# Kernel optimization log

Hardware: AMD Instinct MI355X
Metric: run time of the kernel (lower is better)

Reference implementation:

```python
import jax, jax.numpy as jnp
import numpy as np

N, E, D, R = 50000, 800000, 64, 65


def setup_inputs() -> dict:
    key = jax.random.key(0)
    ks = jax.random.split(key, 8)
    x = jax.random.normal(ks[0], (N, D), dtype=jnp.float32)
    src = jax.random.randint(ks[1], (E,), 0, N, dtype=jnp.int32)
    dst = jax.random.randint(ks[2], (E,), 0, N, dtype=jnp.int32)
    edge_type = jax.random.randint(ks[3], (E,), 0, R, dtype=jnp.int32)
    s = 1.0 / np.sqrt(D)
    W1 = jax.random.normal(ks[4], (R, D, D), dtype=jnp.float32) * s
    Wl1 = jax.random.normal(ks[5], (D, D), dtype=jnp.float32) * s
    W2 = jax.random.normal(ks[6], (R, D, D), dtype=jnp.float32) * s
    Wl2 = jax.random.normal(ks[7], (D, D), dtype=jnp.float32) * s
    return {"x": x, "src": src, "dst": dst, "edge_type": edge_type,
            "W1": W1, "Wl1": Wl1, "W2": W2, "Wl2": Wl2}


def _rgcn_layer(x, src, dst, edge_type, W, Wl):
    # x: [N, D_in], W: [R, D_in, D_out], Wl: [D_in, D_out]
    n = x.shape[0]
    r = W.shape[0]
    # per-relation transform of all node features: [R, N, D_out]
    xw = jnp.einsum('nd,rdh->rnh', x, W)
    # gather transformed source feature for each edge by its relation: [E, D_out]
    msg = xw[edge_type, src]
    # mean aggregation per (destination node, relation) as in PyG RGCNConv
    key = dst.astype(jnp.int32) * r + edge_type
    cnt = jax.ops.segment_sum(jnp.ones(key.shape, x.dtype), key, num_segments=n * r)
    norm = 1.0 / jnp.maximum(cnt[key], 1.0)  # [E]
    agg = jax.ops.segment_sum(msg * norm[:, None], dst, num_segments=n)  # [N, D_out]
    # self-loop linear term (self_loop_weights in original module)
    out = agg + x @ Wl
    # activation; dropout is identity in eval mode; batch norm disabled
    return jax.nn.relu(out)


def reference(x, src, dst, edge_type, W1, Wl1, W2, Wl2):
    h = _rgcn_layer(x, src, dst, edge_type, W1, Wl1)
    h = _rgcn_layer(h, src, dst, edge_type, W2, Wl2)
    return h
```

## Files before the change

kernel.cpp:

```cpp
#include <hip/hip_runtime.h>

typedef __attribute__((ext_vector_type(8))) short bf16x8;
typedef __attribute__((ext_vector_type(4))) float f32x4;

constexpr int D = 64;
constexpr int SEG = 64;
constexpr int CSTR = 16;
constexpr int TSTR = 68;

__device__ inline unsigned short f2bf(float f) {
  unsigned u = __float_as_uint(f);
  u += 0x7fff + ((u >> 16) & 1);
  return (unsigned short)(u >> 16);
}
__device__ inline float bflo(unsigned u) { return __uint_as_float(u << 16); }
__device__ inline float bfhi(unsigned u) { return __uint_as_float(u & 0xffff0000u); }

__global__ __launch_bounds__(256) void count_kernel(
    const int* __restrict__ dst, const int* __restrict__ et,
    int* __restrict__ bcnt, int* __restrict__ deg, int E, int R, int nbE) {
  __shared__ int lh[128];
  int t = threadIdx.x;
  if (t < 128) lh[t] = 0;
  __syncthreads();
  int e = blockIdx.x * 256 + t;
  if (e < E) {
    atomicAdd(&deg[(long)dst[e] * CSTR], 1);
    atomicAdd(&lh[et[e]], 1);
  }
  __syncthreads();
  if (t < R) bcnt[t * nbE + blockIdx.x] = lh[t];
}

__global__ __launch_bounds__(256) void scanA_dual_kernel(
    const int* __restrict__ bcnt, const int* __restrict__ deg,
    int* __restrict__ bsum, int nBC, int N, int nbBC) {
  __shared__ int s[256];
  int t = threadIdx.x;
  int b = blockIdx.x;
  int v;
  if (b < nbBC) {
    int i = b * 256 + t;
    v = (i < nBC) ? bcnt[i] : 0;
  } else {
    int i = (b - nbBC) * 256 + t;
    v = (i < N) ? deg[(long)i * CSTR] : 0;
  }
  s[t] = v;
  __syncthreads();
  for (int o = 128; o > 0; o >>= 1) {
    if (t < o) s[t] += s[t + o];
    __syncthreads();
  }
  if (t == 0) bsum[b] = s[0];
}

__device__ inline void scanB_region(int* bsum, int nb, int t) {
  __shared__ int s[256];
  __shared__ int carry;
  if (t == 0) carry = 0;
  __syncthreads();
  for (int base = 0; base < nb; base += 256) {
    int i = base + t;
    int v = (i < nb) ? bsum[i] : 0;
    s[t] = v;
    __syncthreads();
    for (int o = 1; o < 256; o <<= 1) {
      int u = (t >= o) ? s[t - o] : 0;
      __syncthreads();
      s[t] += u;
      __syncthreads();
    }
    if (i < nb) bsum[i] = carry + s[t] - v;
    __syncthreads();
    if (t == 0) carry += s[255];
    __syncthreads();
  }
}

__global__ __launch_bounds__(256) void scanB_dual_kernel(
    int* __restrict__ bsum, int nbBC, int nbN) {
  int t = threadIdx.x;
  scanB_region(bsum, nbBC, t);
  scanB_region(bsum + nbBC, nbN, t);
}

__global__ __launch_bounds__(256) void scanC_dual_kernel(
    const int* __restrict__ bcnt, const int* __restrict__ deg,
    const int* __restrict__ bsum, int* __restrict__ prefE,
    int* __restrict__ dstoff, int* __restrict__ cur2,
    int nBC, int N, int nbBC) {
  __shared__ int s[256];
  int t = threadIdx.x;
  int b = blockIdx.x;
  bool isBC = (b < nbBC);
  int i = (isBC ? b : b - nbBC) * 256 + t;
  int n = isBC ? nBC : N;
  int v = 0;
  if (i < n) v = isBC ? bcnt[i] : deg[(long)i * CSTR];
  s[t] = v;
  __syncthreads();
  for (int o = 1; o < 256; o <<= 1) {
    int u = (t >= o) ? s[t - o] : 0;
    __syncthreads();
    s[t] += u;
    __syncthreads();
  }
  int excl = bsum[b] + s[t] - v;
  if (isBC) {
    if (i < n) prefE[i] = excl;
    if (i == n - 1) prefE[n] = excl + v;
  } else {
    if (i < n) { dstoff[i] = excl; cur2[(long)i * CSTR] = excl; }
    if (i == n - 1) dstoff[n] = excl + v;
  }
}

__global__ void prefix_wrel_kernel(const int* __restrict__ prefE,
                                   int* __restrict__ cursor, int* __restrict__ wrel,
                                   int nbE, int R) {
  __shared__ int sc[128];
  int l = threadIdx.x;
  int c = 0;
  if (l < R) {
    int tot = prefE[(l + 1) * nbE] - prefE[l * nbE];
    c = (tot + SEG - 1) & ~(SEG - 1);
  }
  sc[l] = c;
  __syncthreads();
  for (int ofs = 1; ofs < 128; ofs <<= 1) {
    int v = (l >= ofs) ? sc[l - ofs] : 0;
    __syncthreads();
    sc[l] += v;
    __syncthreads();
  }
  if (l < R) {
    int cur = sc[l] - c;
    cursor[l] = cur;
    int w0 = cur >> 6;
    int nw = c >> 6;
    for (int w = 0; w < nw; ++w) wrel[w0 + w] = l;
  }
}

__global__ __launch_bounds__(256) void scatter_kernel(
    const int* __restrict__ src, const int* __restrict__ dst, const int* __restrict__ et,
    const int* __restrict__ cursor, const int* __restrict__ prefE,
    int* __restrict__ cur2, int2* __restrict__ eidx,
    int E, int R, int nbE) {
  __shared__ int lh[128];
  __shared__ int lbase[128];
  int t = threadIdx.x, b = blockIdx.x;
  if (t < R) {
    lh[t] = 0;
    lbase[t] = cursor[t] + prefE[t * nbE + b] - prefE[t * nbE];
  }
  __syncthreads();
  int e = b * 256 + t;
  if (e < E) {
    int r = et[e], s = src[e], d = dst[e];
    int lr = atomicAdd(&lh[r], 1);
    int jd = atomicAdd(&cur2[(long)d * CSTR], 1);
    int pos = lbase[r] + lr;
    eidx[pos] = make_int2(s, jd);
  }
}

__global__ __launch_bounds__(256) void cvt_all_kernel(
    const float* __restrict__ x, unsigned short* __restrict__ xb, int nx,
    const float* __restrict__ W1, unsigned short* __restrict__ WT1,
    const float* __restrict__ W2, unsigned short* __restrict__ WT2, int nw,
    const float* __restrict__ Wl1, unsigned short* __restrict__ WTl1,
    const float* __restrict__ Wl2, unsigned short* __restrict__ WTl2, int nl) {
  int i = blockIdx.x * 256 + threadIdx.x;
  if (i < nx) { xb[i] = f2bf(x[i]); return; }
  i -= nx;
  if (i < 2 * nw) {
    const float* W = (i < nw) ? W1 : W2;
    unsigned short* WT = (i < nw) ? WT1 : WT2;
    int i2 = (i < nw) ? i : i - nw;
    int n = i2 & 63, k = (i2 >> 6) & 63, r = i2 >> 12;
    WT[(r << 12) + (n << 6) + k] = f2bf(W[(r << 12) + (k << 6) + n]);
    return;
  }
  i -= 2 * nw;
  if (i < 2 * nl) {
    const float* W = (i < nl) ? Wl1 : Wl2;
    unsigned short* WT = (i < nl) ? WTl1 : WTl2;
    int i2 = (i < nl) ? i : i - nl;
    int n = i2 & 63, k = (i2 >> 6) & 63;
    WT[(n << 6) + k] = f2bf(W[(k << 6) + n]);
  }
}

__global__ __launch_bounds__(256) __attribute__((amdgpu_waves_per_eu(1, 4)))
void msg_kernel(const unsigned short* __restrict__ xb,
                const unsigned short* __restrict__ WT,
                const int2* __restrict__ eidx, const int* __restrict__ wrel,
                unsigned int* __restrict__ msgp, int* __restrict__ relrow, int nwaves) {
  const int lane = (int)threadIdx.x & 63;
  const int l15 = lane & 15;
  const int q = lane >> 4;
  const int wave = blockIdx.x * 4 + ((int)threadIdx.x >> 6);
  if (wave >= nwaves) return;
  const long base = (long)wave * SEG;
  const int r = wrel[wave];
  const unsigned short* wb = WT + ((long)r << 12);
  bf16x8 Bf[4][2];
#pragma unroll
  for (int nt = 0; nt < 4; ++nt)
#pragma unroll
    for (int kh = 0; kh < 2; ++kh)
      Bf[nt][kh] = *(const bf16x8*)(wb + (nt * 16 + l15) * 64 + kh * 32 + q * 8);
#pragma unroll
  for (int t = 0; t < 4; ++t) {
    int2 rec = eidx[base + t * 16 + l15];
    if (relrow && lane < 16 && rec.y >= 0) relrow[rec.y] = r;
    const unsigned short* xr = xb + ((long)max(rec.x, 0) << 6);
    bf16x8 A0 = *(const bf16x8*)(xr + q * 8);
    bf16x8 A1 = *(const bf16x8*)(xr + 32 + q * 8);
    f32x4 acc0 = (f32x4)0.0f, acc1 = (f32x4)0.0f, acc2 = (f32x4)0.0f, acc3 = (f32x4)0.0f;
    acc0 = __builtin_amdgcn_mfma_f32_16x16x32_bf16(A0, Bf[0][0], acc0, 0, 0, 0);
    acc0 = __builtin_amdgcn_mfma_f32_16x16x32_bf16(A1, Bf[0][1], acc0, 0, 0, 0);
    acc1 = __builtin_amdgcn_mfma_f32_16x16x32_bf16(A0, Bf[1][0], acc1, 0, 0, 0);
    acc1 = __builtin_amdgcn_mfma_f32_16x16x32_bf16(A1, Bf[1][1], acc1, 0, 0, 0);
    acc2 = __builtin_amdgcn_mfma_f32_16x16x32_bf16(A0, Bf[2][0], acc2, 0, 0, 0);
    acc2 = __builtin_amdgcn_mfma_f32_16x16x32_bf16(A1, Bf[2][1], acc2, 0, 0, 0);
    acc3 = __builtin_amdgcn_mfma_f32_16x16x32_bf16(A0, Bf[3][0], acc3, 0, 0, 0);
    acc3 = __builtin_amdgcn_mfma_f32_16x16x32_bf16(A1, Bf[3][1], acc3, 0, 0, 0);
#pragma unroll
    for (int rg = 0; rg < 4; ++rg) {
      int row = q * 4 + rg;
      int jd = __shfl(rec.y, row);
      if (jd >= 0) {
        unsigned p0 = (unsigned)f2bf(acc0[rg]) | ((unsigned)f2bf(acc1[rg]) << 16);
        unsigned p1 = (unsigned)f2bf(acc2[rg]) | ((unsigned)f2bf(acc3[rg]) << 16);
        unsigned int* mp = msgp + (long)jd * 32;
        mp[l15] = p0;
        mp[16 + l15] = p1;
      }
    }
  }
}

__global__ __launch_bounds__(256) void aggself_kernel(
    const unsigned int* __restrict__ msgp, const int* __restrict__ dstoff,
    const int* __restrict__ relrow, const unsigned short* __restrict__ xbin,
    const unsigned short* __restrict__ WTl, float* __restrict__ out,
    unsigned short* __restrict__ hb, int N) {
  __shared__ float tile[4][16 * TSTR];
  __shared__ int rsh[4][256];
  __shared__ float fsh[4][256];
  const int wv = (int)threadIdx.x >> 6;
  const int lane = (int)threadIdx.x & 63;
  const int j = lane & 31;
  const int half = lane >> 5;
  const int l15 = lane & 15;
  const int q = lane >> 4;
  const int base = blockIdx.x * 64 + wv * 16;
  bf16x8 Bf[4][2];
#pragma unroll
  for (int nt = 0; nt < 4; ++nt)
#pragma unroll
    for (int kh = 0; kh < 2; ++kh)
      Bf[nt][kh] = *(const bf16x8*)(WTl + (nt * 16 + l15) * 64 + kh * 32 + q * 8);
  if (base >= N) return;
  for (int k = 0; k < 16; ++k) {
    int d = base + k;
    float aLo = 0.f, aHi = 0.f;
    if (d < N) {
      const int off = dstoff[d], end = dstoff[d + 1];
      const int deg = end - off;
      if (deg > 0 && deg <= 256) {
        const int nit = (deg + 63) >> 6;
        int cl[4];
        for (int it = 0; it < nit; ++it) {
          int l = it * 64 + lane;
          if (l < deg) rsh[wv][l] = relrow[off + l];
        }
        __threadfence_block();
        for (int it = 0; it < nit; ++it) {
          int l = it * 64 + lane;
          if (l < deg) {
            int rv = rsh[wv][l];
            int c = 0;
            for (int m = 0; m < deg; ++m) c += (rsh[wv][m] == rv) ? 1 : 0;
            cl[it] = c;
          }
        }
        for (int it = 0; it < nit; ++it) {
          int l = it * 64 + lane;
          if (l < deg) fsh[wv][l] = 1.0f / (float)cl[it];
        }
        __threadfence_block();
        float a0 = 0.f, a1 = 0.f, b0 = 0.f, b1 = 0.f;
        int i = off + half;
        for (; i + 2 < end; i += 4) {
          float w0 = fsh[wv][i - off];
          float w1 = fsh[wv][i + 2 - off];
          unsigned u0 = msgp[(long)i * 32 + j];
          unsigned u1 = msgp[(long)(i + 2) * 32 + j];
          a0 = fmaf(w0, bflo(u0), a0);
          a1 = fmaf(w0, bfhi(u0), a1);
          b0 = fmaf(w1, bflo(u1), b0);
          b1 = fmaf(w1, bfhi(u1), b1);
        }
        if (i < end) {
          float w0 = fsh[wv][i - off];
          unsigned u0 = msgp[(long)i * 32 + j];
          a0 = fmaf(w0, bflo(u0), a0);
          a1 = fmaf(w0, bfhi(u0), a1);
        }
        aLo = a0 + b0;
        aHi = a1 + b1;
      } else if (deg > 256) {
        for (int i = off + half; i < end; i += 2) {
          int rv = relrow[i];
          int c = 0;
          for (int m = off; m < end; ++m) c += (relrow[m] == rv) ? 1 : 0;
          float w = 1.0f / (float)c;
          unsigned u0 = msgp[(long)i * 32 + j];
          aLo = fmaf(w, bflo(u0), aLo);
          aHi = fmaf(w, bfhi(u0), aHi);
        }
      }
    }
    aLo += __shfl_xor(aLo, 32);
    aHi += __shfl_xor(aHi, 32);
    if (half == 0) {
      int colLo = (j < 16) ? j : j + 16;
      tile[wv][k * TSTR + colLo] = aLo;
      tile[wv][k * TSTR + colLo + 16] = aHi;
    }
  }
  __threadfence_block();
  const int m = min(base + l15, N - 1);
  const unsigned short* xr = xbin + ((long)m << 6);
  bf16x8 A0 = *(const bf16x8*)(xr + q * 8);
  bf16x8 A1 = *(const bf16x8*)(xr + 32 + q * 8);
  f32x4 acc[4];
#pragma unroll
  for (int nt = 0; nt < 4; ++nt) {
#pragma unroll
    for (int rg = 0; rg < 4; ++rg)
      acc[nt][rg] = tile[wv][(q * 4 + rg) * TSTR + nt * 16 + l15];
  }
#pragma unroll
  for (int nt = 0; nt < 4; ++nt) {
    acc[nt] = __builtin_amdgcn_mfma_f32_16x16x32_bf16(A0, Bf[nt][0], acc[nt], 0, 0, 0);
    acc[nt] = __builtin_amdgcn_mfma_f32_16x16x32_bf16(A1, Bf[nt][1], acc[nt], 0, 0, 0);
  }
#pragma unroll
  for (int rg = 0; rg < 4; ++rg) {
    int node = base + q * 4 + rg;
    if (node < N) {
#pragma unroll
      for (int nt = 0; nt < 4; ++nt) {
        float v = fmaxf(acc[nt][rg], 0.0f);
        out[(long)node * D + nt * 16 + l15] = v;
        if (hb) hb[(long)node * D + nt * 16 + l15] = f2bf(v);
      }
    }
  }
}

extern "C" void kernel_launch(void* const* d_in, const int* in_sizes, int n_in,
                              void* d_out, int out_size, void* d_ws, size_t ws_size,
                              hipStream_t stream) {
  const float* x   = (const float*)d_in[0];
  const int* src   = (const int*)d_in[1];
  const int* dst   = (const int*)d_in[2];
  const int* et    = (const int*)d_in[3];
  const float* W1  = (const float*)d_in[4];
  const float* Wl1 = (const float*)d_in[5];
  const float* W2  = (const float*)d_in[6];
  const float* Wl2 = (const float*)d_in[7];
  float* out = (float*)d_out;

  const int N = in_sizes[0] / D;
  const int E = in_sizes[1];
  const int R = in_sizes[4] / (D * D);

  const int Ecap = ((E + SEG - 1) & ~(SEG - 1)) + R * SEG;
  const int nwaves = Ecap / SEG;
  const int nbN = (N + 255) / 256;
  const int nbE = (E + 255) / 256;
  const int nBC = R * nbE;
  const int nbBC = (nBC + 255) / 256;

  char* ws = (char*)d_ws;
  size_t off = 0;
  auto alloc = [&](size_t bytes) -> void* {
    void* p = (void*)(ws + off);
    off += (bytes + 255) & ~(size_t)255;
    return p;
  };
  int*   cursor = (int*)alloc((size_t)R * sizeof(int));
  int*   deg    = (int*)alloc((size_t)N * CSTR * sizeof(int));
  int*   cur2   = (int*)alloc((size_t)N * CSTR * sizeof(int));
  int*   bcnt   = (int*)alloc((size_t)nBC * sizeof(int));
  int*   prefE  = (int*)alloc((size_t)(nBC + 1) * sizeof(int));
  int*   bsum   = (int*)alloc((size_t)(nbBC + nbN) * sizeof(int));
  int*   dstoff = (int*)alloc((size_t)(N + 1) * sizeof(int));
  int*   relrow = (int*)alloc((size_t)E * sizeof(int));
  int*   wrel   = (int*)alloc((size_t)nwaves * sizeof(int));
  int2*  eidx   = (int2*)alloc((size_t)(Ecap + SEG) * sizeof(int2));
  unsigned int* msgp = (unsigned int*)alloc((size_t)E * 32 * sizeof(unsigned int));
  unsigned short* xb  = (unsigned short*)alloc((size_t)N * D * sizeof(unsigned short));
  unsigned short* hb  = (unsigned short*)alloc((size_t)N * D * sizeof(unsigned short));
  unsigned short* WT1 = (unsigned short*)alloc((size_t)R * D * D * sizeof(unsigned short));
  unsigned short* WT2 = (unsigned short*)alloc((size_t)R * D * D * sizeof(unsigned short));
  unsigned short* WTl1 = (unsigned short*)alloc((size_t)D * D * sizeof(unsigned short));
  unsigned short* WTl2 = (unsigned short*)alloc((size_t)D * D * sizeof(unsigned short));
  (void)ws_size; (void)n_in; (void)out_size;

  const int msg_blocks = (nwaves + 3) / 4;
  const int as_blocks = (N + 63) / 64;
  const int nx = N * D;
  const int nw = R * D * D;
  const int nl = D * D;
  const int cvt_total = nx + 2 * nw + 2 * nl;

  hipMemsetAsync(deg, 0, (size_t)N * CSTR * sizeof(int), stream);
  hipMemsetAsync(wrel, 0, (size_t)nwaves * sizeof(int), stream);
  hipMemsetAsync(eidx, 0xFF, (size_t)(Ecap + SEG) * sizeof(int2), stream);
  count_kernel<<<nbE, 256, 0, stream>>>(dst, et, bcnt, deg, E, R, nbE);
  scanA_dual_kernel<<<nbBC + nbN, 256, 0, stream>>>(bcnt, deg, bsum, nBC, N, nbBC);
  scanB_dual_kernel<<<1, 256, 0, stream>>>(bsum, nbBC, nbN);
  scanC_dual_kernel<<<nbBC + nbN, 256, 0, stream>>>(bcnt, deg, bsum, prefE,
                                                    dstoff, cur2, nBC, N, nbBC);
  prefix_wrel_kernel<<<1, 128, 0, stream>>>(prefE, cursor, wrel, nbE, R);
  scatter_kernel<<<nbE, 256, 0, stream>>>(src, dst, et, cursor, prefE, cur2,
                                          eidx, E, R, nbE);
  cvt_all_kernel<<<(cvt_total + 255) / 256, 256, 0, stream>>>(
      x, xb, nx, W1, WT1, W2, WT2, nw, Wl1, WTl1, Wl2, WTl2, nl);

  msg_kernel<<<msg_blocks, 256, 0, stream>>>(xb, WT1, eidx, wrel, msgp, relrow, nwaves);
  aggself_kernel<<<as_blocks, 256, 0, stream>>>(msgp, dstoff, relrow, xb, WTl1,
                                                out, hb, N);
  msg_kernel<<<msg_blocks, 256, 0, stream>>>(hb, WT2, eidx, wrel, msgp, nullptr, nwaves);
  aggself_kernel<<<as_blocks, 256, 0, stream>>>(msgp, dstoff, relrow, hb, WTl2,
                                                out, nullptr, N);
}
```

Measured before the change: 392.6 us.

## Split fused aggregate+selfloop into weight, aggregation and selfloop kernels

Replaces the fused aggregation/self-loop kernel with three kernels. A weight kernel computes per-edge mean-normalisation factors once and reuses them in both layers. A per-node aggregation kernel gives each destination node its own wave instead of 16 nodes serialised per wave, and a separate MFMA self-loop kernel reads the aggregate back from global memory. This exposes more parallelism and removes the duplicated count work in layer two, at the cost of an extra float N×D round trip through memory and more launches. It also drops the waves_per_eu hint on msg_kernel.

```diff
diff --git a/kernel.cpp b/kernel.cpp
--- a/kernel.cpp
+++ b/kernel.cpp
@@ -6,7 +6,6 @@
 constexpr int D = 64;
 constexpr int SEG = 64;
 constexpr int CSTR = 16;
-constexpr int TSTR = 68;
 
 __device__ inline unsigned short f2bf(float f) {
   unsigned u = __float_as_uint(f);
@@ -193,7 +192,7 @@
   }
 }
 
-__global__ __launch_bounds__(256) __attribute__((amdgpu_waves_per_eu(1, 4)))
+__global__ __launch_bounds__(256)
 void msg_kernel(const unsigned short* __restrict__ xb,
                 const unsigned short* __restrict__ WT,
                 const int2* __restrict__ eidx, const int* __restrict__ wrel,
@@ -243,122 +242,128 @@
   }
 }
 
-__global__ __launch_bounds__(256) void aggself_kernel(
+__global__ __launch_bounds__(256) void weight_kernel(
+    const int* __restrict__ relrow, const int* __restrict__ dstoff,
+    float* __restrict__ wrow, int N) {
+  __shared__ int rsh[4][256];
+  const int wv = (int)threadIdx.x >> 6;
+  const int lane = (int)threadIdx.x & 63;
+  const int d = blockIdx.x * 4 + wv;
+  if (d >= N) return;
+  const int off = dstoff[d], end = dstoff[d + 1];
+  const int deg = end - off;
+  if (deg <= 0) return;
+  if (deg <= 256) {
+    const int nit = (deg + 63) >> 6;
+    for (int it = 0; it < nit; ++it) {
+      int l = it * 64 + lane;
+      if (l < deg) rsh[wv][l] = relrow[off + l];
+    }
+    __threadfence_block();
+    for (int it = 0; it < nit; ++it) {
+      int l = it * 64 + lane;
+      if (l < deg) {
+        int rv = rsh[wv][l];
+        int c = 0;
+        for (int m = 0; m < deg; ++m) c += (rsh[wv][m] == rv) ? 1 : 0;
+        wrow[off + l] = 1.0f / (float)c;
+      }
+    }
+  } else {
+    for (int l = lane; l < deg; l += 64) {
+      int rv = relrow[off + l];
+      int c = 0;
+      for (int m = off; m < end; ++m) c += (relrow[m] == rv) ? 1 : 0;
+      wrow[off + l] = 1.0f / (float)c;
+    }
+  }
+}
+
+__global__ __launch_bounds__(256) void agg_kernel(
     const unsigned int* __restrict__ msgp, const int* __restrict__ dstoff,
-    const int* __restrict__ relrow, const unsigned short* __restrict__ xbin,
-    const unsigned short* __restrict__ WTl, float* __restrict__ out,
-    unsigned short* __restrict__ hb, int N) {
-  __shared__ float tile[4][16 * TSTR];
-  __shared__ int rsh[4][256];
-  __shared__ float fsh[4][256];
-  const int wv = (int)threadIdx.x >> 6;
+    const float* __restrict__ wrow, float* __restrict__ agg, int N) {
   const int lane = (int)threadIdx.x & 63;
   const int j = lane & 31;
   const int half = lane >> 5;
+  const int d = blockIdx.x * 4 + ((int)threadIdx.x >> 6);
+  if (d >= N) return;
+  const int off = dstoff[d], end = dstoff[d + 1];
+  float a0 = 0.f, a1 = 0.f, b0 = 0.f, b1 = 0.f;
+  int i = off + half;
+  for (; i + 2 < end; i += 4) {
+    float w0 = wrow[i];
+    float w1 = wrow[i + 2];
+    unsigned u0 = msgp[(long)i * 32 + j];
+    unsigned u1 = msgp[(long)(i + 2) * 32 + j];
+    a0 = fmaf(w0, bflo(u0), a0);
+    a1 = fmaf(w0, bfhi(u0), a1);
+    b0 = fmaf(w1, bflo(u1), b0);
+    b1 = fmaf(w1, bfhi(u1), b1);
+  }
+  if (i < end) {
+    float w0 = wrow[i];
+    unsigned u0 = msgp[(long)i * 32 + j];
+    a0 = fmaf(w0, bflo(u0), a0);
+    a1 = fmaf(w0, bfhi(u0), a1);
+  }
+  float aLo = a0 + b0, aHi = a1 + b1;
+  aLo += __shfl_xor(aLo, 32);
+  aHi += __shfl_xor(aHi, 32);
+  if (half == 0) {
+    int colLo = (j < 16) ? j : j + 16;
+    agg[(long)d * D + colLo] = aLo;
+    agg[(long)d * D + colLo + 16] = aHi;
+  }
+}
+
+__global__ __launch_bounds__(256) void selfloop_kernel(
+    const unsigned short* __restrict__ xbin, const unsigned short* __restrict__ WTl,
+    const float* __restrict__ agg, float* __restrict__ out,
+    unsigned short* __restrict__ hb, int N) {
+  const int lane = (int)threadIdx.x & 63;
   const int l15 = lane & 15;
   const int q = lane >> 4;
-  const int base = blockIdx.x * 64 + wv * 16;
+  const int wave = blockIdx.x * 4 + ((int)threadIdx.x >> 6);
+  const int base = wave * 64;
+  if (base >= N) return;
   bf16x8 Bf[4][2];
 #pragma unroll
   for (int nt = 0; nt < 4; ++nt)
 #pragma unroll
     for (int kh = 0; kh < 2; ++kh)
       Bf[nt][kh] = *(const bf16x8*)(WTl + (nt * 16 + l15) * 64 + kh * 32 + q * 8);
-  if (base >= N) return;
-  for (int k = 0; k < 16; ++k) {
-    int d = base + k;
-    float aLo = 0.f, aHi = 0.f;
-    if (d < N) {
-      const int off = dstoff[d], end = dstoff[d + 1];
-      const int deg = end - off;
-      if (deg > 0 && deg <= 256) {
-        const int nit = (deg + 63) >> 6;
-        int cl[4];
-        for (int it = 0; it < nit; ++it) {
-          int l = it * 64 + lane;
-          if (l < deg) rsh[wv][l] = relrow[off + l];
+#pragma unroll
+  for (int t = 0; t < 4; ++t) {
+    const int row0 = base + t * 16;
+    if (row0 >= N) break;
+    const int m = min(row0 + l15, N - 1);
+    const unsigned short* xr = xbin + ((long)m << 6);
+    bf16x8 A0 = *(const bf16x8*)(xr + q * 8);
+    bf16x8 A1 = *(const bf16x8*)(xr + 32 + q * 8);
+    f32x4 acc[4];
+#pragma unroll
+    for (int nt = 0; nt < 4; ++nt) {
+#pragma unroll
+      for (int rg = 0; rg < 4; ++rg) {
+        int node = row0 + q * 4 + rg;
+        acc[nt][rg] = (node < N) ? agg[(long)node * D + nt * 16 + l15] : 0.0f;
+      }
+    }
+#pragma unroll
+    for (int nt = 0; nt < 4; ++nt) {
+      acc[nt] = __builtin_amdgcn_mfma_f32_16x16x32_bf16(A0, Bf[nt][0], acc[nt], 0, 0, 0);
+      acc[nt] = __builtin_amdgcn_mfma_f32_16x16x32_bf16(A1, Bf[nt][1], acc[nt], 0, 0, 0);
+    }
+#pragma unroll
+    for (int rg = 0; rg < 4; ++rg) {
+      int node = row0 + q * 4 + rg;
+      if (node < N) {
+#pragma unroll
+        for (int nt = 0; nt < 4; ++nt) {
+          float v = fmaxf(acc[nt][rg], 0.0f);
+          out[(long)node * D + nt * 16 + l15] = v;
+          if (hb) hb[(long)node * D + nt * 16 + l15] = f2bf(v);
         }
-        __threadfence_block();
-        for (int it = 0; it < nit; ++it) {
-          int l = it * 64 + lane;
-          if (l < deg) {
-            int rv = rsh[wv][l];
-            int c = 0;
-            for (int m = 0; m < deg; ++m) c += (rsh[wv][m] == rv) ? 1 : 0;
-            cl[it] = c;
-          }
-        }
-        for (int it = 0; it < nit; ++it) {
-          int l = it * 64 + lane;
-          if (l < deg) fsh[wv][l] = 1.0f / (float)cl[it];
-        }
-        __threadfence_block();
-        float a0 = 0.f, a1 = 0.f, b0 = 0.f, b1 = 0.f;
-        int i = off + half;
-        for (; i + 2 < end; i += 4) {
-          float w0 = fsh[wv][i - off];
-          float w1 = fsh[wv][i + 2 - off];
-          unsigned u0 = msgp[(long)i * 32 + j];
-          unsigned u1 = msgp[(long)(i + 2) * 32 + j];
-          a0 = fmaf(w0, bflo(u0), a0);
-          a1 = fmaf(w0, bfhi(u0), a1);
-          b0 = fmaf(w1, bflo(u1), b0);
-          b1 = fmaf(w1, bfhi(u1), b1);
-        }
-        if (i < end) {
-          float w0 = fsh[wv][i - off];
-          unsigned u0 = msgp[(long)i * 32 + j];
-          a0 = fmaf(w0, bflo(u0), a0);
-          a1 = fmaf(w0, bfhi(u0), a1);
-        }
-        aLo = a0 + b0;
-        aHi = a1 + b1;
-      } else if (deg > 256) {
-        for (int i = off + half; i < end; i += 2) {
-          int rv = relrow[i];
-          int c = 0;
-          for (int m = off; m < end; ++m) c += (relrow[m] == rv) ? 1 : 0;
-          float w = 1.0f / (float)c;
-          unsigned u0 = msgp[(long)i * 32 + j];
-          aLo = fmaf(w, bflo(u0), aLo);
-          aHi = fmaf(w, bfhi(u0), aHi);
-        }
-      }
-    }
-    aLo += __shfl_xor(aLo, 32);
-    aHi += __shfl_xor(aHi, 32);
-    if (half == 0) {
-      int colLo = (j < 16) ? j : j + 16;
-      tile[wv][k * TSTR + colLo] = aLo;
-      tile[wv][k * TSTR + colLo + 16] = aHi;
-    }
-  }
-  __threadfence_block();
-  const int m = min(base + l15, N - 1);
-  const unsigned short* xr = xbin + ((long)m << 6);
-  bf16x8 A0 = *(const bf16x8*)(xr + q * 8);
-  bf16x8 A1 = *(const bf16x8*)(xr + 32 + q * 8);
-  f32x4 acc[4];
-#pragma unroll
-  for (int nt = 0; nt < 4; ++nt) {
-#pragma unroll
-    for (int rg = 0; rg < 4; ++rg)
-      acc[nt][rg] = tile[wv][(q * 4 + rg) * TSTR + nt * 16 + l15];
-  }
-#pragma unroll
-  for (int nt = 0; nt < 4; ++nt) {
-    acc[nt] = __builtin_amdgcn_mfma_f32_16x16x32_bf16(A0, Bf[nt][0], acc[nt], 0, 0, 0);
-    acc[nt] = __builtin_amdgcn_mfma_f32_16x16x32_bf16(A1, Bf[nt][1], acc[nt], 0, 0, 0);
-  }
-#pragma unroll
-  for (int rg = 0; rg < 4; ++rg) {
-    int node = base + q * 4 + rg;
-    if (node < N) {
-#pragma unroll
-      for (int nt = 0; nt < 4; ++nt) {
-        float v = fmaxf(acc[nt][rg], 0.0f);
-        out[(long)node * D + nt * 16 + l15] = v;
-        if (hb) hb[(long)node * D + nt * 16 + l15] = f2bf(v);
       }
     }
   }
@@ -403,9 +408,11 @@
   int*   bsum   = (int*)alloc((size_t)(nbBC + nbN) * sizeof(int));
   int*   dstoff = (int*)alloc((size_t)(N + 1) * sizeof(int));
   int*   relrow = (int*)alloc((size_t)E * sizeof(int));
+  float* wrow   = (float*)alloc((size_t)E * sizeof(float));
   int*   wrel   = (int*)alloc((size_t)nwaves * sizeof(int));
   int2*  eidx   = (int2*)alloc((size_t)(Ecap + SEG) * sizeof(int2));
   unsigned int* msgp = (unsigned int*)alloc((size_t)E * 32 * sizeof(unsigned int));
+  float* agg    = (float*)alloc((size_t)N * D * sizeof(float));
   unsigned short* xb  = (unsigned short*)alloc((size_t)N * D * sizeof(unsigned short));
   unsigned short* hb  = (unsigned short*)alloc((size_t)N * D * sizeof(unsigned short));
   unsigned short* WT1 = (unsigned short*)alloc((size_t)R * D * D * sizeof(unsigned short));
@@ -415,7 +422,8 @@
   (void)ws_size; (void)n_in; (void)out_size;
 
   const int msg_blocks = (nwaves + 3) / 4;
-  const int as_blocks = (N + 63) / 64;
+  const int agg_blocks = (N + 3) / 4;
+  const int sl_blocks = ((N + 63) / 64 + 3) / 4;
   const int nx = N * D;
   const int nw = R * D * D;
   const int nl = D * D;
@@ -436,9 +444,11 @@
       x, xb, nx, W1, WT1, W2, WT2, nw, Wl1, WTl1, Wl2, WTl2, nl);
 
   msg_kernel<<<msg_blocks, 256, 0, stream>>>(xb, WT1, eidx, wrel, msgp, relrow, nwaves);
-  aggself_kernel<<<as_blocks, 256, 0, stream>>>(msgp, dstoff, relrow, xb, WTl1,
-                                                out, hb, N);
+  weight_kernel<<<agg_blocks, 256, 0, stream>>>(relrow, dstoff, wrow, N);
+  agg_kernel<<<agg_blocks, 256, 0, stream>>>(msgp, dstoff, wrow, agg, N);
+  selfloop_kernel<<<sl_blocks, 256, 0, stream>>>(xb, WTl1, agg, out, hb, N);
+
   msg_kernel<<<msg_blocks, 256, 0, stream>>>(hb, WT2, eidx, wrel, msgp, nullptr, nwaves);
-  aggself_kernel<<<as_blocks, 256, 0, stream>>>(msgp, dstoff, relrow, hb, WTl2,
-                                                out, nullptr, N);
-}
+  agg_kernel<<<agg_blocks, 256, 0, stream>>>(msgp, dstoff, wrow, agg, N);
+  selfloop_kernel<<<sl_blocks, 256, 0, stream>>>(hb, WTl2, agg, out, nullptr, N);
+}
```

After: 337.3 us. 1.16x faster.
